# Optimization experiments

Hardware: AMD Instinct MI355X
Metric: run time of the kernel (lower is better)

## Reference

```python
import jax, jax.numpy as jnp
import numpy as np

TIME_BATCH = 10
BASE_MU = 1.0
BASE_MU_BIAS = 1.0
C = 1.0
T, I, O = 10240, 2048, 1024


def setup_inputs() -> dict:
    key = jax.random.key(0)
    k1, k2, k3, k4 = jax.random.split(key, 4)
    input_psp = jax.random.uniform(k1, (T, I), dtype=jnp.float32)
    output_spikes = (jax.random.uniform(k2, (T, O)) < 0.02).astype(jnp.float32)
    weights = jax.random.normal(k3, (O, I), dtype=jnp.float32)
    biases = jax.random.normal(k4, (O,), dtype=jnp.float32)
    N_k = jnp.ones((O, 1), dtype=jnp.float32)
    return {"input_psp": input_psp, "output_spikes": output_spikes,
            "weights": weights, "biases": biases, "N_k": N_k}


def reference(input_psp, output_spikes, weights, biases, N_k):
    time_steps = input_psp.shape[0]
    iters = time_steps // TIME_BATCH
    # (iters, tb, I) / (iters, tb, O)
    psp_b = input_psp.reshape(iters, TIME_BATCH, -1)
    spk_b = output_spikes.reshape(iters, TIME_BATCH, -1)
    tos = spk_b.sum(axis=1)           # (iters, O) total spikes per output neuron per time-batch
    toss = tos.sum(axis=1)            # (iters,)   total spikes per time-batch

    def step(carry, xs):
        w, b, nk = carry
        psp, spk, tos_i, toss_i = xs
        # correlation for this time-batch: (O, I). Same math as the
        # precomputed einsum 't...o,t...i->toi' indexed at i, but computed
        # inside the scan to avoid materializing an (iters, O, I) tensor.
        corr = jnp.einsum('to,ti->oi', spk, psp)
        mu_w = BASE_MU / nk                      # (O, 1), uses nk BEFORE update
        mu_b = BASE_MU_BIAS / jnp.sum(nk)        # scalar
        dw = corr * C * jnp.exp(-w) - tos_i[:, None]
        db = (jnp.exp(-b) * tos_i - 1.0) * toss_i
        w = w + mu_w * dw
        b = b + mu_b * db
        nk = nk + tos_i[:, None]
        return (w, b, nk), None

    (w_f, b_f, nk_f), _ = jax.lax.scan(step, (weights, biases, N_k),
                                       (psp_b, spk_b, tos, toss))
    return (w_f, b_f)
```

## Files before the change

### kernel.cpp

```cpp
#include <hip/hip_runtime.h>
#include <cstdint>
#include <cstddef>

#define I_DIM   2048
#define O_DIM   1024
#define TB      10
#define ITERS   1024
#define I4      512
#define LISTMAX 320
#define LSTRIDE 336
#define LOG2E   1.44269504088896340736f
#define LN2     0.69314718055994530942f

#define EXP2_HW(x) __builtin_amdgcn_exp2f(x)

__global__ __launch_bounds__(256)
void prep_kernel(const float* __restrict__ spk,
                 unsigned short* __restrict__ mask_T,
                 float* __restrict__ toss) {
    const int t   = blockIdx.x;
    const int tid = threadIdx.x;
    const float4* base4 = (const float4*)(spk + (size_t)t * TB * O_DIM);
    float    s[4] = {0.f, 0.f, 0.f, 0.f};
    unsigned m[4] = {0u, 0u, 0u, 0u};
#pragma unroll
    for (int i = 0; i < TB; ++i) {
        float4 v = base4[(size_t)i * (O_DIM / 4) + tid];
        s[0] += v.x; if (v.x != 0.f) m[0] |= (1u << i);
        s[1] += v.y; if (v.y != 0.f) m[1] |= (1u << i);
        s[2] += v.z; if (v.z != 0.f) m[2] |= (1u << i);
        s[3] += v.w; if (v.w != 0.f) m[3] |= (1u << i);
    }
#pragma unroll
    for (int j = 0; j < 4; ++j)
        mask_T[(size_t)(tid * 4 + j) * ITERS + t] = (unsigned short)m[j];
    __shared__ float red[256];
    red[tid] = s[0] + s[1] + s[2] + s[3];
    __syncthreads();
    for (int st = 128; st > 0; st >>= 1) {
        if (tid < st) red[tid] += red[tid + st];
        __syncthreads();
    }
    if (tid == 0) toss[t] = red[0];
}

__global__ __launch_bounds__(256)
void compact_bias_kernel(const unsigned short* __restrict__ mask_T,
                         const float* __restrict__ toss,
                         const float* __restrict__ Nk,
                         const float* __restrict__ b_in,
                         uint2* __restrict__ lists,
                         int* __restrict__ counts,
                         float* __restrict__ b_out) {
    __shared__ float s_h[ITERS];
    __shared__ float red[256];
    const int tid = threadIdx.x;
    if (blockIdx.x < 256) {
        const int o    = blockIdx.x * 4 + (tid >> 6);
        const int lane = tid & 63;
        const unsigned short* row = mask_T + (size_t)o * ITERS;
        uint2* list = lists + (size_t)o * LSTRIDE;
        const float nk0 = Nk[o];
        int cnt = 0, tot = 0;
        for (int base = 0; base < ITERS; base += 64) {
            unsigned int m = row[base + lane];
            bool act = (m != 0u);
            int tos = __popc(m);
            int v = tos;
#pragma unroll
            for (int d = 1; d < 64; d <<= 1) {
                int y = __shfl_up(v, d);
                if (lane >= d) v += y;
            }
            const int excl = v - tos;
            unsigned long long b = __ballot(act);
            int pre = __popcll(b & ((1ull << lane) - 1ull));
            if (act && cnt + pre < LISTMAX) {
                float nk_k = nk0 + (float)(tot + excl);
                float inv  = __builtin_amdgcn_rcpf(nk_k) * LOG2E;
                unsigned s0   = (unsigned)(__ffs(m) - 1);
                unsigned row0 = (unsigned)(base + lane) * TB + s0;
                unsigned info = row0 | (s0 << 14) | ((m & (m - 1)) << 18)
                              | ((unsigned)tos << 28);
                list[cnt + pre] = make_uint2(info, __float_as_uint(-inv));
            }
            cnt += __popcll(b);
            tot += __shfl(v, 63);
        }
        if (lane < 8) {
            int c = cnt < LISTMAX ? cnt : LISTMAX;
            if (lane == 0) counts[o] = c;
            list[c + lane] = make_uint2(0u, 0u);
        }
    } else {
        float s = 0.f;
        for (int i = tid; i < O_DIM; i += 256) s += Nk[i];
        red[tid] = s;
        __syncthreads();
        for (int st = 128; st > 0; st >>= 1) {
            if (tid < st) red[tid] += red[tid + st];
            __syncthreads();
        }
        const float snk0 = red[0];
        __syncthreads();

        const int t0 = tid * 4;
        const float4 tv = ((const float4*)toss)[tid];
        red[tid] = tv.x + tv.y + tv.z + tv.w;
        __syncthreads();
        for (int d = 1; d < 256; d <<= 1) {
            float add = (tid >= d) ? red[tid - d] : 0.f;
            __syncthreads();
            red[tid] += add;
            __syncthreads();
        }
        const float base = (tid ? red[tid - 1] : 0.f) + snk0;
        s_h[t0]     = LOG2E * tv.x * __builtin_amdgcn_rcpf(base);
        s_h[t0 + 1] = LOG2E * tv.y * __builtin_amdgcn_rcpf(base + tv.x);
        s_h[t0 + 2] = LOG2E * tv.z * __builtin_amdgcn_rcpf(base + tv.x + tv.y);
        s_h[t0 + 3] = LOG2E * tv.w * __builtin_amdgcn_rcpf(base + tv.x + tv.y + tv.z);
        __syncthreads();

        const int o = (blockIdx.x - 256) * 256 + tid;
        float bs = b_in[o] * LOG2E;
        const uint4* row4 = (const uint4*)(mask_T + (size_t)o * ITERS);
        for (int blk = 0; blk < ITERS / 8; ++blk) {
            uint4 v = row4[blk];
            unsigned wds[4] = {v.x, v.y, v.z, v.w};
#pragma unroll
            for (int j = 0; j < 8; ++j) {
                unsigned m = (wds[j >> 1] >> ((j & 1) * 16)) & 0xFFFFu;
                float tos_t = (float)__popc(m);
                float h = s_h[blk * 8 + j];
                float e = EXP2_HW(-bs);
                bs = __builtin_fmaf(h * tos_t, e, bs) - h;
            }
        }
        b_out[o] = bs * LN2;
    }
}

__global__ __launch_bounds__(256)
void stdp_main_kernel(const float* __restrict__ psp,
                      const float* __restrict__ w_in,
                      const uint2* __restrict__ lists,
                      const int* __restrict__ counts,
                      float* __restrict__ w_out) {
    const int bid  = blockIdx.x;
    const int seg  = bid & 7;
    const int wv   = __builtin_amdgcn_readfirstlane(threadIdx.x >> 6);
    const int lane = threadIdx.x & 63;
    const int o    = ((bid >> 3) << 2) | wv;
    const int lane4 = seg * 64 + lane;

    const float4* __restrict__ psp4 = (const float4*)psp + lane4;
    float4 w0 = ((const float4*)w_in)[(size_t)o * I4 + lane4];
    float4 n = make_float4(w0.x * -LOG2E, w0.y * -LOG2E,
                           w0.z * -LOG2E, w0.w * -LOG2E);

    const uint2* lp = lists + (size_t)o * LSTRIDE;
    const int count = counts[o];

    auto rowof = [&](unsigned ex) -> float4 {
        return psp4[(size_t)(ex & 0x3FFFu) << 9];
    };

    if (count > 0) {
        uint4 A = *(const uint4*)(lp + 0);
        uint4 B = *(const uint4*)(lp + 2);
        uint4 C = *(const uint4*)(lp + 4);
        float4 p0 = rowof(A.x), p1 = rowof(A.z);
        float4 p2 = rowof(B.x), p3 = rowof(B.z);

        for (int k = 0; k < count; k += 2) {
            const uint4 D = *(const uint4*)(lp + k + 6);
            const float4 p4 = rowof(C.x), p5 = rowof(C.z);

            {
                float4 c = p0;
                unsigned rem = (A.x >> 18) & 0x3FFu;
                if (rem) {
                    unsigned t10 = (A.x & 0x3FFFu) - ((A.x >> 14) & 0xFu);
                    do {
                        int sbit = __ffs(rem) - 1;
                        rem &= rem - 1;
                        const float4 q = psp4[(size_t)(t10 + sbit) << 9];
                        c.x += q.x; c.y += q.y; c.z += q.z; c.w += q.w;
                    } while (rem);
                }
                const float ninv = __uint_as_float(A.y);
                const float tosf = (float)(A.x >> 28);
                float t, s;
                t = EXP2_HW(n.x); s = __builtin_fmaf(c.x, t, -tosf); n.x = __builtin_fmaf(ninv, s, n.x);
                t = EXP2_HW(n.y); s = __builtin_fmaf(c.y, t, -tosf); n.y = __builtin_fmaf(ninv, s, n.y);
                t = EXP2_HW(n.z); s = __builtin_fmaf(c.z, t, -tosf); n.z = __builtin_fmaf(ninv, s, n.z);
                t = EXP2_HW(n.w); s = __builtin_fmaf(c.w, t, -tosf); n.w = __builtin_fmaf(ninv, s, n.w);
            }
            {
                float4 c = p1;
                unsigned rem = (A.z >> 18) & 0x3FFu;
                if (rem) {
                    unsigned t10 = (A.z & 0x3FFFu) - ((A.z >> 14) & 0xFu);
                    do {
                        int sbit = __ffs(rem) - 1;
                        rem &= rem - 1;
                        const float4 q = psp4[(size_t)(t10 + sbit) << 9];
                        c.x += q.x; c.y += q.y; c.z += q.z; c.w += q.w;
                    } while (rem);
                }
                const float ninv = __uint_as_float(A.w);
                const float tosf = (float)(A.z >> 28);
                float t, s;
                t = EXP2_HW(n.x); s = __builtin_fmaf(c.x, t, -tosf); n.x = __builtin_fmaf(ninv, s, n.x);
                t = EXP2_HW(n.y); s = __builtin_fmaf(c.y, t, -tosf); n.y = __builtin_fmaf(ninv, s, n.y);
                t = EXP2_HW(n.z); s = __builtin_fmaf(c.z, t, -tosf); n.z = __builtin_fmaf(ninv, s, n.z);
                t = EXP2_HW(n.w); s = __builtin_fmaf(c.w, t, -tosf); n.w = __builtin_fmaf(ninv, s, n.w);
            }

            A = B; B = C; C = D;
            p0 = p2; p1 = p3; p2 = p4; p3 = p5;
        }
    }

    float4 ov = make_float4(n.x * -LN2, n.y * -LN2, n.z * -LN2, n.w * -LN2);
    ((float4*)w_out)[(size_t)o * I4 + lane4] = ov;
}

extern "C" void kernel_launch(void* const* d_in, const int* in_sizes, int n_in,
                              void* d_out, int out_size, void* d_ws, size_t ws_size,
                              hipStream_t stream) {
    const float* psp = (const float*)d_in[0];
    const float* spk = (const float*)d_in[1];
    const float* w   = (const float*)d_in[2];
    const float* b   = (const float*)d_in[3];
    const float* Nk  = (const float*)d_in[4];

    float* w_out = (float*)d_out;
    float* b_out = (float*)d_out + (size_t)O_DIM * I_DIM;

    char* ws = (char*)d_ws;
    unsigned short* mask_T = (unsigned short*)ws;
    uint2*          lists  = (uint2*)(ws + (size_t)O_DIM * ITERS * 2);
    int*            counts = (int*)(ws + (size_t)O_DIM * ITERS * 2
                                       + (size_t)O_DIM * LSTRIDE * 8);
    float*          toss   = (float*)(counts + O_DIM);

    prep_kernel<<<ITERS, 256, 0, stream>>>(spk, mask_T, toss);
    compact_bias_kernel<<<260, 256, 0, stream>>>(mask_T, toss, Nk, b,
                                                 lists, counts, b_out);
    stdp_main_kernel<<<O_DIM / 4 * 8, 256, 0, stream>>>(psp, w, lists, counts, w_out);
}
```

Before: 130.4 us.

## Flatten spike lists to one entry per spike with carried partial sums

The compaction kernel now writes one list entry per spike instead of one per active time-batch. Entries for earlier spikes in a batch carry an accumulate flag and a zero step size, and the main kernel carries their psp rows into the next entry through a pending sum. This removes the data-dependent inner loop of serially issued extra psp loads, so every row load goes through the existing software prefetch. In exchange, batches with several spikes add entries that each do wasted exp2 and FMA work, and lists grow slightly longer.

```diff
diff --git a/kernel.cpp b/kernel.cpp
--- a/kernel.cpp
+++ b/kernel.cpp
@@ -9,6 +9,7 @@
 #define I4      512
 #define LISTMAX 320
 #define LSTRIDE 336
+#define ACCUMF  0x8000u
 #define LOG2E   1.44269504088896340736f
 #define LN2     0.69314718055994530942f
 
@@ -61,10 +62,9 @@
         const unsigned short* row = mask_T + (size_t)o * ITERS;
         uint2* list = lists + (size_t)o * LSTRIDE;
         const float nk0 = Nk[o];
-        int cnt = 0, tot = 0;
+        int tot = 0;
         for (int base = 0; base < ITERS; base += 64) {
             unsigned int m = row[base + lane];
-            bool act = (m != 0u);
             int tos = __popc(m);
             int v = tos;
 #pragma unroll
@@ -73,22 +73,29 @@
                 if (lane >= d) v += y;
             }
             const int excl = v - tos;
-            unsigned long long b = __ballot(act);
-            int pre = __popcll(b & ((1ull << lane) - 1ull));
-            if (act && cnt + pre < LISTMAX) {
+            if (m) {
                 float nk_k = nk0 + (float)(tot + excl);
                 float inv  = __builtin_amdgcn_rcpf(nk_k) * LOG2E;
-                unsigned s0   = (unsigned)(__ffs(m) - 1);
-                unsigned row0 = (unsigned)(base + lane) * TB + s0;
-                unsigned info = row0 | (s0 << 14) | ((m & (m - 1)) << 18)
-                              | ((unsigned)tos << 28);
-                list[cnt + pre] = make_uint2(info, __float_as_uint(-inv));
-            }
-            cnt += __popcll(b);
+                unsigned t10 = (unsigned)(base + lane) * TB;
+                int pos = tot + excl;
+                unsigned mm = m;
+                while (mm) {
+                    int s = __ffs(mm) - 1;
+                    mm &= mm - 1;
+                    if (pos < LISTMAX) {
+                        if (mm)
+                            list[pos] = make_uint2((t10 + s) | ACCUMF, 0u);
+                        else
+                            list[pos] = make_uint2((t10 + s) | ((unsigned)tos << 28),
+                                                   __float_as_uint(-inv));
+                    }
+                    ++pos;
+                }
+            }
             tot += __shfl(v, 63);
         }
         if (lane < 8) {
-            int c = cnt < LISTMAX ? cnt : LISTMAX;
+            int c = tot < LISTMAX ? tot : LISTMAX;
             if (lane == 0) counts[o] = c;
             list[c + lane] = make_uint2(0u, 0u);
         }
@@ -157,8 +164,10 @@
     float4 w0 = ((const float4*)w_in)[(size_t)o * I4 + lane4];
     float4 n = make_float4(w0.x * -LOG2E, w0.y * -LOG2E,
                            w0.z * -LOG2E, w0.w * -LOG2E);
-
-    const uint2* lp = lists + (size_t)o * LSTRIDE;
+    float4 cpend = make_float4(0.f, 0.f, 0.f, 0.f);
+
+    const uint2* lp  = lists + (size_t)o * LSTRIDE;
+    const uint4* lp4 = (const uint4*)lp;
     const int count = counts[o];
 
     auto rowof = [&](unsigned ex) -> float4 {
@@ -166,28 +175,19 @@
     };
 
     if (count > 0) {
-        uint4 A = *(const uint4*)(lp + 0);
-        uint4 B = *(const uint4*)(lp + 2);
-        uint4 C = *(const uint4*)(lp + 4);
+        uint4 A = lp4[0];
+        uint4 B = lp4[1];
+        uint4 C = lp4[2];
         float4 p0 = rowof(A.x), p1 = rowof(A.z);
         float4 p2 = rowof(B.x), p3 = rowof(B.z);
 
         for (int k = 0; k < count; k += 2) {
-            const uint4 D = *(const uint4*)(lp + k + 6);
+            const uint4 D = lp4[(k >> 1) + 3];
             const float4 p4 = rowof(C.x), p5 = rowof(C.z);
 
             {
-                float4 c = p0;
-                unsigned rem = (A.x >> 18) & 0x3FFu;
-                if (rem) {
-                    unsigned t10 = (A.x & 0x3FFFu) - ((A.x >> 14) & 0xFu);
-                    do {
-                        int sbit = __ffs(rem) - 1;
-                        rem &= rem - 1;
-                        const float4 q = psp4[(size_t)(t10 + sbit) << 9];
-                        c.x += q.x; c.y += q.y; c.z += q.z; c.w += q.w;
-                    } while (rem);
-                }
+                float4 c = make_float4(p0.x + cpend.x, p0.y + cpend.y,
+                                       p0.z + cpend.z, p0.w + cpend.w);
                 const float ninv = __uint_as_float(A.y);
                 const float tosf = (float)(A.x >> 28);
                 float t, s;
@@ -195,19 +195,13 @@
                 t = EXP2_HW(n.y); s = __builtin_fmaf(c.y, t, -tosf); n.y = __builtin_fmaf(ninv, s, n.y);
                 t = EXP2_HW(n.z); s = __builtin_fmaf(c.z, t, -tosf); n.z = __builtin_fmaf(ninv, s, n.z);
                 t = EXP2_HW(n.w); s = __builtin_fmaf(c.w, t, -tosf); n.w = __builtin_fmaf(ninv, s, n.w);
+                const bool acc = (A.x & ACCUMF) != 0u;
+                cpend.x = acc ? c.x : 0.f; cpend.y = acc ? c.y : 0.f;
+                cpend.z = acc ? c.z : 0.f; cpend.w = acc ? c.w : 0.f;
             }
             {
-                float4 c = p1;
-                unsigned rem = (A.z >> 18) & 0x3FFu;
-                if (rem) {
-                    unsigned t10 = (A.z & 0x3FFFu) - ((A.z >> 14) & 0xFu);
-                    do {
-                        int sbit = __ffs(rem) - 1;
-                        rem &= rem - 1;
-                        const float4 q = psp4[(size_t)(t10 + sbit) << 9];
-                        c.x += q.x; c.y += q.y; c.z += q.z; c.w += q.w;
-                    } while (rem);
-                }
+                float4 c = make_float4(p1.x + cpend.x, p1.y + cpend.y,
+                                       p1.z + cpend.z, p1.w + cpend.w);
                 const float ninv = __uint_as_float(A.w);
                 const float tosf = (float)(A.z >> 28);
                 float t, s;
@@ -215,6 +209,9 @@
                 t = EXP2_HW(n.y); s = __builtin_fmaf(c.y, t, -tosf); n.y = __builtin_fmaf(ninv, s, n.y);
                 t = EXP2_HW(n.z); s = __builtin_fmaf(c.z, t, -tosf); n.z = __builtin_fmaf(ninv, s, n.z);
                 t = EXP2_HW(n.w); s = __builtin_fmaf(c.w, t, -tosf); n.w = __builtin_fmaf(ninv, s, n.w);
+                const bool acc = (A.z & ACCUMF) != 0u;
+                cpend.x = acc ? c.x : 0.f; cpend.y = acc ? c.y : 0.f;
+                cpend.z = acc ? c.z : 0.f; cpend.w = acc ? c.w : 0.f;
             }
 
             A = B; B = C; C = D;
```

Result: slower. 145.7 us (+11.8%).
